# Optimization experiments

Hardware: AMD Instinct MI355X
Metric: run time of the kernel (lower is better)

Reference implementation:

```python
import jax, jax.numpy as jnp
import numpy as np

SFREQ = 100
NPERSEG = 100  # min(n_times=200, 100)
NOVERLAP = NPERSEG // 2

# periodic hann window (scipy get_window('hann', N) with sym=False)
_WIN_NP = 0.5 - 0.5 * np.cos(2.0 * np.pi * np.arange(NPERSEG) / NPERSEG)
_WIN_SQ_SUM = float(np.sum(_WIN_NP ** 2))
_FREQS = np.fft.rfftfreq(NPERSEG, 1.0 / SFREQ)  # 0..50 Hz, 51 bins
_BANDS = [(0.5, 4.0), (4.0, 8.0), (8.0, 13.0), (13.0, 30.0)]  # delta/theta/alpha/beta
_BAND_IDX = [np.where((_FREQS >= lo) & (_FREQS <= hi))[0] for lo, hi in _BANDS]


def welch_band_features(x):
    """Batched Welch PSD band powers. x: (B,C,T) -> (B, C*4)."""
    B, C, T = x.shape
    step = NPERSEG - NOVERLAP
    n_seg = (T - NPERSEG) // step + 1
    seg_idx = np.arange(n_seg)[:, None] * step + np.arange(NPERSEG)  # (S, L)
    segs = x[..., seg_idx]                              # (B,C,S,L)
    segs = segs - segs.mean(-1, keepdims=True)          # detrend='constant'
    win = jnp.asarray(_WIN_NP, x.dtype)
    spec = jnp.fft.rfft(segs * win, axis=-1)            # (B,C,S,F)
    scale = 1.0 / (SFREQ * _WIN_SQ_SUM)
    psd = (spec.real ** 2 + spec.imag ** 2) * scale
    psd = psd.at[..., 1:-1].multiply(2.0)               # one-sided, nfft even
    psd = psd.mean(-2)                                  # average over segments -> (B,C,F)
    feats = jnp.stack([psd[..., idx].mean(-1) for idx in _BAND_IDX], axis=-1)  # (B,C,4)
    return feats.reshape(B, C * 4)


def setup_inputs() -> dict:
    key = jax.random.key(0)
    ks = jax.random.split(key, 16)
    B, C, T = 2048, 129, 200
    red = C // 8  # 16
    s = 0.05
    inp = {
        "x": jax.random.normal(ks[0], (B, C, T), jnp.float32),
        # channel attention fc (no bias)
        "w_att1": jax.random.normal(ks[1], (C, red), jnp.float32) * s,
        "w_att2": jax.random.normal(ks[2], (red, C), jnp.float32) * s,
        # stand-in EEGNeX backbone: time-mean pool + linear C->64
        "w_bb": jax.random.normal(ks[3], (C, 64), jnp.float32) * s,
        "b_bb": jnp.zeros((64,), jnp.float32),
        # freq encoder
        "w_fe1": jax.random.normal(ks[4], (C * 4, 128), jnp.float32) * s,
        "b_fe1": jnp.zeros((128,), jnp.float32),
        "w_fe2": jax.random.normal(ks[5], (128, 64), jnp.float32) * s,
        "b_fe2": jnp.zeros((64,), jnp.float32),
        # head
        "w_h1": jax.random.normal(ks[6], (128, 128), jnp.float32) * s,
        "b_h1": jnp.zeros((128,), jnp.float32),
        "w_h2": jax.random.normal(ks[7], (128, 64), jnp.float32) * s,
        "b_h2": jnp.zeros((64,), jnp.float32),
        "w_h3": jax.random.normal(ks[8], (64, 1), jnp.float32) * s,
        "b_h3": jnp.zeros((1,), jnp.float32),
    }
    return inp


def reference(x, w_att1, w_att2, w_bb, b_bb, w_fe1, b_fe1, w_fe2, b_fe2,
              w_h1, b_h1, w_h2, b_h2, w_h3, b_h3):
    # --- channel attention ---
    avg = x.mean(-1)                                    # (B,C)
    mx = x.max(-1)                                      # (B,C)
    fc = lambda v: jax.nn.relu(v @ w_att1) @ w_att2
    att = jax.nn.sigmoid(fc(avg) + fc(mx))[..., None]   # (B,C,1)
    x_att = x * att
    # --- backbone (stand-in for EEGNeXBase): time pool + linear ---
    time_feat = jax.nn.relu(x_att.mean(-1) @ w_bb + b_bb)  # (B,64)
    # --- frequency branch (computed from raw x, detached in original) ---
    freq = welch_band_features(jax.lax.stop_gradient(x))   # (B, C*4)
    freq = jax.nn.relu(freq @ w_fe1 + b_fe1)
    freq = jax.nn.relu(freq @ w_fe2 + b_fe2)               # (B,64)
    # --- head ---
    h = jnp.concatenate([time_feat, freq], axis=1)         # (B,128)
    h = jax.nn.relu(h @ w_h1 + b_h1)
    h = jax.nn.relu(h @ w_h2 + b_h2)
    return h @ w_h3 + b_h3                                  # (B,1)
```

## Files before the change

kernel.cpp:

```cpp
#include <hip/hip_runtime.h>
#include <math.h>

constexpr int BB = 2048;
constexpr int CC = 129;
constexpr int TT = 200;
constexpr int NPAIR = BB * CC;
constexpr int NPG   = NPAIR / 16;
constexpr int NBLK  = NPG / 4;
constexpr int XSTR  = 204;
constexpr int WSLICE = 16 * XSTR;

constexpr int OFF_AVG = 8192;
constexpr int OFF_MX  = OFF_AVG + NPAIR;
constexpr int OFF_FT  = OFF_MX + NPAIR;

typedef __bf16 bf16x8 __attribute__((ext_vector_type(8)));
typedef float  f32x4  __attribute__((ext_vector_type(4)));

union BFU { int4 v; bf16x8 b; };
union BSU { __bf16 b; unsigned short u; };

__global__ void kInit(unsigned short* __restrict__ bfr) {
    int tid = blockIdx.x * 256 + threadIdx.x;
    if (tid >= 16384) return;
    int i    = tid & 7;
    int lane = (tid >> 3) & 63;
    int h    = (tid >> 9) & 1;
    int nt   = (tid >> 10) & 3;
    int ks   = tid >> 12;
    int k = ks * 32 + (lane >> 4) * 8 + i;
    int n = nt * 16 + (lane & 15);
    float v = 0.f;
    if (k < 100) {
        if (n < 60) {
            int kb = (n >> 1) + 1;
            const float C = 0.06283185307179587f;
            float w = 0.5f - 0.5f * cosf(C * (float)k);
            int ph = (kb * k) % 100;
            float ang = C * (float)ph;
            v = w * ((n & 1) ? sinf(ang) : cosf(ang));
        } else if (n == 60) {
            v = 0.01f;
        }
    }
    __bf16 hb = (__bf16)v;
    BSU out;
    if (h == 0) out.b = hb;
    else        out.b = (__bf16)(v - (float)hb);
    bfr[tid] = out.u;
}

__global__ __launch_bounds__(256, 3) void kA(const float* __restrict__ x,
                                             const unsigned short* __restrict__ bfr,
                                             float* __restrict__ avg,
                                             float* __restrict__ mxg,
                                             float* __restrict__ feat) {
    __shared__ __align__(16) float xs[4 * WSLICE];

    const int tid  = threadIdx.x;
    const int wv   = tid >> 6;
    const int lane = tid & 63;
    const int pg   = blockIdx.x * 4 + wv;
    const int quad = lane >> 4, mrow = lane & 15;
    float* wx = xs + wv * WSLICE;

    {
        const float4* xg = (const float4*)(x + (size_t)pg * 16 * TT);
        #pragma unroll
        for (int it = 0; it < 13; it++) {
            int idx = lane + it * 64;
            if (idx < 800) {
                float4 v = xg[idx];
                int p = idx / 50, t4 = (idx % 50) * 4;
                *(float4*)(wx + p * XSTR + t4) = v;
            }
        }
    }

    f32x4 acc[3][4];
    #pragma unroll
    for (int a = 0; a < 3; a++)
        #pragma unroll
        for (int b = 0; b < 4; b++) acc[a][b] = f32x4{0.f, 0.f, 0.f, 0.f};

    float m = -3.4e38f;
    const int4* bg = (const int4*)bfr;
    const float* rbase = wx + mrow * XSTR;

    #pragma unroll 1
    for (int ks = 0; ks < 4; ks++) {
        bf16x8 Th[4], Tl[4];
        #pragma unroll
        for (int nt = 0; nt < 4; nt++) {
            BFU uh, ul;
            uh.v = bg[((ks * 4 + nt) * 2 + 0) * 64 + lane];
            ul.v = bg[((ks * 4 + nt) * 2 + 1) * 64 + lane];
            Th[nt] = uh.b;
            Tl[nt] = ul.b;
        }
        #pragma unroll
        for (int sg = 0; sg < 3; sg++) {
            float f[8];
            if (ks < 3) {
                const float* s = rbase + sg * 50 + ks * 32 + quad * 8;
                float2 f0 = *(const float2*)(s);
                float2 f1 = *(const float2*)(s + 2);
                float2 f2 = *(const float2*)(s + 4);
                float2 f3 = *(const float2*)(s + 6);
                f[0] = f0.x; f[1] = f0.y; f[2] = f1.x; f[3] = f1.y;
                f[4] = f2.x; f[5] = f2.y; f[6] = f3.x; f[7] = f3.y;
                if (sg != 1) {
                    m = fmaxf(m, fmaxf(fmaxf(f[0], f[1]), fmaxf(f[2], f[3])));
                    m = fmaxf(m, fmaxf(fmaxf(f[4], f[5]), fmaxf(f[6], f[7])));
                }
            } else {
                const float* s = rbase + sg * 50 + 96;
                float2 f0 = *(const float2*)(s);
                float2 f1 = *(const float2*)(s + 2);
                if (sg != 1)
                    m = fmaxf(m, fmaxf(fmaxf(f0.x, f0.y), fmaxf(f1.x, f1.y)));
                bool v0 = (quad == 0);
                f[0] = v0 ? f0.x : 0.f; f[1] = v0 ? f0.y : 0.f;
                f[2] = v0 ? f1.x : 0.f; f[3] = v0 ? f1.y : 0.f;
                f[4] = 0.f; f[5] = 0.f; f[6] = 0.f; f[7] = 0.f;
            }
            bf16x8 Xh, Xl;
            #pragma unroll
            for (int i = 0; i < 8; i++) {
                __bf16 hb = (__bf16)f[i];
                Xh[i] = hb;
                Xl[i] = (__bf16)(f[i] - (float)hb);
            }
            __builtin_amdgcn_s_setprio(1);
            #pragma unroll
            for (int nt = 0; nt < 4; nt++) {
                acc[sg][nt] = __builtin_amdgcn_mfma_f32_16x16x32_bf16(Th[nt], Xl, acc[sg][nt], 0, 0, 0);
                acc[sg][nt] = __builtin_amdgcn_mfma_f32_16x16x32_bf16(Tl[nt], Xh, acc[sg][nt], 0, 0, 0);
                acc[sg][nt] = __builtin_amdgcn_mfma_f32_16x16x32_bf16(Th[nt], Xh, acc[sg][nt], 0, 0, 0);
            }
            __builtin_amdgcn_s_setprio(0);
        }
    }

    float s0 = 0.f, s1 = 0.f, s2 = 0.f, s3 = 0.f;
    float mu0 = 0.f, mu2 = 0.f;
    #pragma unroll
    for (int sg = 0; sg < 3; sg++) {
        float mu = __shfl(acc[sg][3][0], 48 | mrow, 64);
        if (sg == 0) mu0 = mu;
        if (sg == 2) mu2 = mu;
        #pragma unroll
        for (int nt = 0; nt < 4; nt++) {
            #pragma unroll
            for (int i = 0; i < 4; i++) {
                float v = acc[sg][nt][i];
                if (nt == 0 && i == 0) v += (quad == 0) ? 25.f * mu : 0.f;
                float w = v * v;
                if (nt == 0) {
                    s0 += (quad <= 1) ? w : 0.f;
                    s1 += (quad * 4 + i >= 6) ? w : 0.f;
                    if (i >= 2) s2 += (quad == 3) ? w : 0.f;
                } else if (nt == 1) {
                    s2 += (quad * 4 + i <= 9) ? w : 0.f;
                    s3 += (quad >= 2) ? w : 0.f;
                } else if (nt == 2) {
                    s3 += w;
                } else {
                    s3 += (quad <= 2) ? w : 0.f;
                }
            }
        }
    }
    s0 += __shfl_xor(s0, 16, 64); s1 += __shfl_xor(s1, 16, 64);
    s2 += __shfl_xor(s2, 16, 64); s3 += __shfl_xor(s3, 16, 64);
    s0 += __shfl_xor(s0, 32, 64); s1 += __shfl_xor(s1, 32, 64);
    s2 += __shfl_xor(s2, 32, 64); s3 += __shfl_xor(s3, 32, 64);
    m = fmaxf(m, __shfl_xor(m, 16, 64));
    m = fmaxf(m, __shfl_xor(m, 32, 64));

    if (quad == 0) {
        int pr = pg * 16 + mrow;
        float4 fo;
        fo.x = s0 * (2.f / 45000.f);
        fo.y = s1 * (2.f / 56250.f);
        fo.z = s2 * (2.f / 67500.f);
        fo.w = s3 * (2.f / 202500.f);
        *(float4*)(feat + (size_t)pr * 4) = fo;
        avg[pr] = (mu0 + mu2) * 0.5f;
        mxg[pr] = m;
    }
}

__global__ __launch_bounds__(256, 8) void kB(const float* __restrict__ avg,
                                             const float* __restrict__ mxv,
                                             const float* __restrict__ feat,
                                             const float* __restrict__ w_att1,
                                             const float* __restrict__ w_att2,
                                             const float* __restrict__ w_bb,
                                             const float* __restrict__ b_bb,
                                             const float* __restrict__ w_fe1,
                                             const float* __restrict__ b_fe1,
                                             const float* __restrict__ w_fe2,
                                             const float* __restrict__ b_fe2,
                                             const float* __restrict__ w_h1,
                                             const float* __restrict__ b_h1,
                                             const float* __restrict__ w_h2,
                                             const float* __restrict__ b_h2,
                                             const float* __restrict__ w_h3,
                                             const float* __restrict__ b_h3,
                                             float* __restrict__ out) {
    __shared__ float s_avg[132], s_mx[132], s_fq[520];
    __shared__ float s_t1a[16], s_t1b[16], s_t1[16];
    __shared__ float s_v[132];
    __shared__ float s_tf[2][64];
    __shared__ float s_p1[2][128];
    __shared__ float s_f1[128];
    __shared__ float s_p2[4][64];
    __shared__ float s_h[128];
    __shared__ float s_pg1[2][128];
    __shared__ float s_g1[128];
    __shared__ float s_pg2[4][64];

    const int b = blockIdx.x;
    const int tid = threadIdx.x;

    for (int i = tid; i < 129; i += 256) { s_avg[i] = avg[b * 129 + i]; s_mx[i] = mxv[b * 129 + i]; }
    for (int i = tid; i < 516; i += 256) s_fq[i] = feat[(size_t)b * 516 + i];
    __syncthreads();

    if (tid < 32) {
        int h = tid & 15;
        const float* src = (tid >= 16) ? s_mx : s_avg;
        float acc = 0.f;
        #pragma unroll 4
        for (int c = 0; c < 129; c++) acc += src[c] * w_att1[c * 16 + h];
        ((tid >= 16) ? s_t1b : s_t1a)[h] = fmaxf(acc, 0.f);
    }
    __syncthreads();
    if (tid < 16) s_t1[tid] = s_t1a[tid] + s_t1b[tid];
    __syncthreads();

    if (tid < 129) {
        float l = 0.f;
        #pragma unroll
        for (int j = 0; j < 16; j++) l += s_t1[j] * w_att2[j * 129 + tid];
        s_v[tid] = s_avg[tid] / (1.f + expf(-l));
    }
    __syncthreads();

    if (tid < 128) {
        int o = tid & 63, ks = tid >> 6;
        int i0 = ks ? 65 : 0, i1 = ks ? 129 : 65;
        float acc = 0.f;
        #pragma unroll 4
        for (int i = i0; i < i1; i++) acc += s_v[i] * w_bb[i * 64 + o];
        s_tf[ks][o] = acc;
    }
    {
        int o = tid & 127, ks = tid >> 7;
        float acc = 0.f;
        #pragma unroll 4
        for (int i = ks * 258; i < ks * 258 + 258; i++) acc += s_fq[i] * w_fe1[i * 128 + o];
        s_p1[ks][o] = acc;
    }
    __syncthreads();
    if (tid < 64) s_h[tid] = fmaxf(s_tf[0][tid] + s_tf[1][tid] + b_bb[tid], 0.f);
    if (tid >= 128) { int o = tid - 128; s_f1[o] = fmaxf(s_p1[0][o] + s_p1[1][o] + b_fe1[o], 0.f); }
    __syncthreads();

    {
        int o = tid & 63, ks = tid >> 6;
        float acc = 0.f;
        #pragma unroll 4
        for (int i = ks * 32; i < ks * 32 + 32; i++) acc += s_f1[i] * w_fe2[i * 64 + o];
        s_p2[ks][o] = acc;
    }
    __syncthreads();
    if (tid < 64) s_h[64 + tid] = fmaxf(s_p2[0][tid] + s_p2[1][tid] + s_p2[2][tid] + s_p2[3][tid] + b_fe2[tid], 0.f);
    __syncthreads();

    {
        int o = tid & 127, ks = tid >> 7;
        float acc = 0.f;
        #pragma unroll 4
        for (int i = ks * 64; i < ks * 64 + 64; i++) acc += s_h[i] * w_h1[i * 128 + o];
        s_pg1[ks][o] = acc;
    }
    __syncthreads();
    if (tid < 128) s_g1[tid] = fmaxf(s_pg1[0][tid] + s_pg1[1][tid] + b_h1[tid], 0.f);
    __syncthreads();

    {
        int o = tid & 63, ks = tid >> 6;
        float acc = 0.f;
        #pragma unroll 4
        for (int i = ks * 32; i < ks * 32 + 32; i++) acc += s_g1[i] * w_h2[i * 64 + o];
        s_pg2[ks][o] = acc;
    }
    __syncthreads();

    if (tid < 64) {
        float g2 = fmaxf(s_pg2[0][tid] + s_pg2[1][tid] + s_pg2[2][tid] + s_pg2[3][tid] + b_h2[tid], 0.f);
        float pz = g2 * w_h3[tid];
        for (int off = 32; off >= 1; off >>= 1) pz += __shfl_xor(pz, off, 64);
        if (tid == 0) out[b] = pz + b_h3[0];
    }
}

extern "C" void kernel_launch(void* const* d_in, const int* in_sizes, int n_in,
                              void* d_out, int out_size, void* d_ws, size_t ws_size,
                              hipStream_t stream) {
    const float* x      = (const float*)d_in[0];
    const float* w_att1 = (const float*)d_in[1];
    const float* w_att2 = (const float*)d_in[2];
    const float* w_bb   = (const float*)d_in[3];
    const float* b_bb   = (const float*)d_in[4];
    const float* w_fe1  = (const float*)d_in[5];
    const float* b_fe1  = (const float*)d_in[6];
    const float* w_fe2  = (const float*)d_in[7];
    const float* b_fe2  = (const float*)d_in[8];
    const float* w_h1   = (const float*)d_in[9];
    const float* b_h1   = (const float*)d_in[10];
    const float* w_h2   = (const float*)d_in[11];
    const float* b_h2   = (const float*)d_in[12];
    const float* w_h3   = (const float*)d_in[13];
    const float* b_h3   = (const float*)d_in[14];

    float* ws = (float*)d_ws;
    unsigned short* bfr = (unsigned short*)ws;
    float* avg  = ws + OFF_AVG;
    float* mxv  = ws + OFF_MX;
    float* feat = ws + OFF_FT;

    kInit<<<64, 256, 0, stream>>>(bfr);
    kA<<<NBLK, 256, 0, stream>>>(x, bfr, avg, mxv, feat);
    kB<<<BB, 256, 0, stream>>>(avg, mxv, feat,
                               w_att1, w_att2, w_bb, b_bb,
                               w_fe1, b_fe1, w_fe2, b_fe2,
                               w_h1, b_h1, w_h2, b_h2, w_h3, b_h3,
                               (float*)d_out);
}
```

Before: 419.1 us.

## Load input tiles straight into LDS with global_load_lds in a chunk-interleaved layout

Replaces the register-staged float4 copy of each wave's 16x200 input slice with direct global-to-LDS loads (global_load_lds, 16 bytes per lane). The LDS layout becomes chunk-interleaved: each 64-float block holds four consecutive floats from each of the 16 rows. All segment reads are remapped to float4 accesses, with the overlapping middle segment reassembled from offset pieces. The first basis-fragment loads are hoisted so they overlap the input transfer. This aims to remove register round-trips and the LDS bank conflicts of the old 204-stride layout, at the cost of fragile index arithmetic.

```diff
diff --git a/kernel.cpp b/kernel.cpp
--- a/kernel.cpp
+++ b/kernel.cpp
@@ -7,8 +7,7 @@
 constexpr int NPAIR = BB * CC;
 constexpr int NPG   = NPAIR / 16;
 constexpr int NBLK  = NPG / 4;
-constexpr int XSTR  = 204;
-constexpr int WSLICE = 16 * XSTR;
+constexpr int WSL   = 3200;
 
 constexpr int OFF_AVG = 8192;
 constexpr int OFF_MX  = OFF_AVG + NPAIR;
@@ -19,6 +18,9 @@
 
 union BFU { int4 v; bf16x8 b; };
 union BSU { __bf16 b; unsigned short u; };
+
+typedef __attribute__((address_space(3))) char  lds_char;
+typedef const __attribute__((address_space(1))) void g_void;
 
 __global__ void kInit(unsigned short* __restrict__ bfr) {
     int tid = blockIdx.x * 256 + threadIdx.x;
@@ -55,26 +57,40 @@
                                              float* __restrict__ avg,
                                              float* __restrict__ mxg,
                                              float* __restrict__ feat) {
-    __shared__ __align__(16) float xs[4 * WSLICE];
+    __shared__ __align__(16) float xs[4 * WSL];
 
     const int tid  = threadIdx.x;
     const int wv   = tid >> 6;
     const int lane = tid & 63;
     const int pg   = blockIdx.x * 4 + wv;
     const int quad = lane >> 4, mrow = lane & 15;
-    float* wx = xs + wv * WSLICE;
-
-    {
-        const float4* xg = (const float4*)(x + (size_t)pg * 16 * TT);
-        #pragma unroll
-        for (int it = 0; it < 13; it++) {
-            int idx = lane + it * 64;
-            if (idx < 800) {
-                float4 v = xg[idx];
-                int p = idx / 50, t4 = (idx % 50) * 4;
-                *(float4*)(wx + p * XSTR + t4) = v;
-            }
-        }
+    float* wx = xs + wv * WSL;
+
+    {
+        const float* gp = x + (size_t)pg * 16 * TT + (lane & 15) * TT + (lane >> 4) * 4;
+        lds_char* lp = (lds_char*)wx;
+        #pragma unroll
+        for (int it = 0; it < 12; it++) {
+            __builtin_amdgcn_global_load_lds((g_void*)(gp + it * 16),
+                                             (__attribute__((address_space(3))) void*)(lp + it * 1024),
+                                             16, 0, 0);
+        }
+        if (lane < 32) {
+            __builtin_amdgcn_global_load_lds((g_void*)(gp + 12 * 16),
+                                             (__attribute__((address_space(3))) void*)(lp + 12 * 1024),
+                                             16, 0, 0);
+        }
+    }
+
+    const int4* bg = (const int4*)bfr;
+    bf16x8 Th[4], Tl[4];
+    #pragma unroll
+    for (int nt = 0; nt < 4; nt++) {
+        BFU uh, ul;
+        uh.v = bg[(nt * 2 + 0) * 64 + lane];
+        ul.v = bg[(nt * 2 + 1) * 64 + lane];
+        Th[nt] = uh.b;
+        Tl[nt] = ul.b;
     }
 
     f32x4 acc[3][4];
@@ -83,45 +99,60 @@
         #pragma unroll
         for (int b = 0; b < 4; b++) acc[a][b] = f32x4{0.f, 0.f, 0.f, 0.f};
 
+    asm volatile("s_waitcnt vmcnt(0)" ::: "memory");
+    __builtin_amdgcn_sched_barrier(0);
+
     float m = -3.4e38f;
-    const int4* bg = (const int4*)bfr;
-    const float* rbase = wx + mrow * XSTR;
+    const float* lbq = wx + mrow * 4 + quad * 128;
+    const float* lb0 = wx + mrow * 4;
 
     #pragma unroll 1
     for (int ks = 0; ks < 4; ks++) {
-        bf16x8 Th[4], Tl[4];
-        #pragma unroll
-        for (int nt = 0; nt < 4; nt++) {
-            BFU uh, ul;
-            uh.v = bg[((ks * 4 + nt) * 2 + 0) * 64 + lane];
-            ul.v = bg[((ks * 4 + nt) * 2 + 1) * 64 + lane];
-            Th[nt] = uh.b;
-            Tl[nt] = ul.b;
+        if (ks > 0) {
+            #pragma unroll
+            for (int nt = 0; nt < 4; nt++) {
+                BFU uh, ul;
+                uh.v = bg[((ks * 4 + nt) * 2 + 0) * 64 + lane];
+                ul.v = bg[((ks * 4 + nt) * 2 + 1) * 64 + lane];
+                Th[nt] = uh.b;
+                Tl[nt] = ul.b;
+            }
         }
         #pragma unroll
         for (int sg = 0; sg < 3; sg++) {
             float f[8];
             if (ks < 3) {
-                const float* s = rbase + sg * 50 + ks * 32 + quad * 8;
-                float2 f0 = *(const float2*)(s);
-                float2 f1 = *(const float2*)(s + 2);
-                float2 f2 = *(const float2*)(s + 4);
-                float2 f3 = *(const float2*)(s + 6);
-                f[0] = f0.x; f[1] = f0.y; f[2] = f1.x; f[3] = f1.y;
-                f[4] = f2.x; f[5] = f2.y; f[6] = f3.x; f[7] = f3.y;
                 if (sg != 1) {
+                    const float* s = ((sg == 0) ? lbq : (lbq + 25 * 64)) + ks * 512;
+                    float4 A  = *(const float4*)(s);
+                    float4 Bv = *(const float4*)(s + 64);
+                    f[0] = A.x;  f[1] = A.y;  f[2] = A.z;  f[3] = A.w;
+                    f[4] = Bv.x; f[5] = Bv.y; f[6] = Bv.z; f[7] = Bv.w;
                     m = fmaxf(m, fmaxf(fmaxf(f[0], f[1]), fmaxf(f[2], f[3])));
                     m = fmaxf(m, fmaxf(fmaxf(f[4], f[5]), fmaxf(f[6], f[7])));
+                } else {
+                    const float* s = lbq + 12 * 64 + ks * 512;
+                    float4 A  = *(const float4*)(s);
+                    float4 Bv = *(const float4*)(s + 64);
+                    float2 Cv = *(const float2*)(s + 128);
+                    f[0] = A.z;  f[1] = A.w;  f[2] = Bv.x; f[3] = Bv.y;
+                    f[4] = Bv.z; f[5] = Bv.w; f[6] = Cv.x; f[7] = Cv.y;
                 }
             } else {
-                const float* s = rbase + sg * 50 + 96;
-                float2 f0 = *(const float2*)(s);
-                float2 f1 = *(const float2*)(s + 2);
-                if (sg != 1)
-                    m = fmaxf(m, fmaxf(fmaxf(f0.x, f0.y), fmaxf(f1.x, f1.y)));
                 bool v0 = (quad == 0);
-                f[0] = v0 ? f0.x : 0.f; f[1] = v0 ? f0.y : 0.f;
-                f[2] = v0 ? f1.x : 0.f; f[3] = v0 ? f1.y : 0.f;
+                if (sg != 1) {
+                    const float* s = lb0 + ((sg == 0) ? 24 : 49) * 64;
+                    float4 A = *(const float4*)(s);
+                    m = fmaxf(m, fmaxf(fmaxf(A.x, A.y), fmaxf(A.z, A.w)));
+                    f[0] = v0 ? A.x : 0.f; f[1] = v0 ? A.y : 0.f;
+                    f[2] = v0 ? A.z : 0.f; f[3] = v0 ? A.w : 0.f;
+                } else {
+                    const float* s = lb0 + 36 * 64;
+                    float4 A  = *(const float4*)(s);
+                    float2 Cv = *(const float2*)(s + 64);
+                    f[0] = v0 ? A.z : 0.f;  f[1] = v0 ? A.w : 0.f;
+                    f[2] = v0 ? Cv.x : 0.f; f[3] = v0 ? Cv.y : 0.f;
+                }
                 f[4] = 0.f; f[5] = 0.f; f[6] = 0.f; f[7] = 0.f;
             }
             bf16x8 Xh, Xl;
```

Result: no change. 415.8 us (-0.8%).
